# Performance work log

Measured on AMD Instinct MI355X. Metric: run time of the kernel, lower is better.

## Reference

```python
import jax, jax.numpy as jnp
import numpy as np

# ---- config (YOLOv4-style, TRAIN_SIZE=608, P2..P5) ----
STRIDES = (4.0, 8.0, 16.0, 32.0)
ANCHORS = np.array([
    [[12, 16], [19, 36], [40, 28], [36, 75]],
    [[36, 75], [76, 55], [72, 146], [142, 110]],
    [[72, 146], [142, 110], [192, 243], [459, 401]],
    [[142, 110], [192, 243], [300, 300], [459, 401]],
], dtype=np.float32)  # [LEVELS, NUM_ANCHORS, 2]
MAX_PROP = 100
SCORE_THRESH = 0.25
IOU_THRESH = 0.5


def decode_prediction(p, anchors, stride):
    # p: [b, A, h, w, 6] -> [b, A*h*w, 5] with xyxy + score
    b, A, h, w, _ = p.shape
    txy, twh, conf, cls = p[..., :2], p[..., 2:4], p[..., 4:5], p[..., 5:6]
    gx, gy = jnp.meshgrid(jnp.arange(w, dtype=p.dtype), jnp.arange(h, dtype=p.dtype))
    grid = jnp.stack([gx, gy], axis=-1)[None, None]  # [1,1,h,w,2]
    xy = (jax.nn.sigmoid(txy) + grid) * stride
    wh = jnp.exp(twh) * anchors[None, :, None, None, :]
    score = jax.nn.sigmoid(conf) * jax.nn.sigmoid(cls)
    x1y1 = xy - 0.5 * wh
    x2y2 = xy + 0.5 * wh
    out = jnp.concatenate([x1y1, x2y2, score], axis=-1)  # [b,A,h,w,5]
    return out.reshape(b, A * h * w, 5)


def _iou_one_vs_all(box, boxes):
    # box: [4], boxes: [N,4] (xyxy)
    lt = jnp.maximum(box[:2], boxes[:, :2])
    rb = jnp.minimum(box[2:], boxes[:, 2:])
    wh = jnp.maximum(rb - lt, 0.0)
    inter = wh[:, 0] * wh[:, 1]
    a1 = jnp.maximum(box[2] - box[0], 0.0) * jnp.maximum(box[3] - box[1], 0.0)
    a2 = jnp.maximum(boxes[:, 2] - boxes[:, 0], 0.0) * jnp.maximum(boxes[:, 3] - boxes[:, 1], 0.0)
    return inter / (a1 + a2 - inter + 1e-9)


def _nms_single(boxes, scores):
    # greedy NMS, padded to MAX_PROP with zero rows
    s0 = jnp.where(scores >= SCORE_THRESH, scores, 0.0)

    def step(s, _):
        i = jnp.argmax(s)
        sc = s[i]
        box = boxes[i]
        keep = sc > 0.0
        row = jnp.where(keep, jnp.concatenate([box, sc[None]]), jnp.zeros(5, boxes.dtype))
        iou = _iou_one_vs_all(box, boxes)
        s = jnp.where((iou > IOU_THRESH) & keep, 0.0, s)
        s = s.at[i].set(0.0)
        return s, row

    _, props = jax.lax.scan(step, s0, None, length=MAX_PROP)
    return props  # [MAX_PROP, 5]


def entry_stop_gradients(t, mask):
    # gradient flows only through entries where mask==1
    return jax.lax.stop_gradient(t) * (1.0 - mask) + t * mask


def _forward(p2, p3, p4, p5):
    anchors = jnp.asarray(ANCHORS)
    d2 = decode_prediction(p2, anchors[0], STRIDES[0])
    d3 = decode_prediction(p3, anchors[1], STRIDES[1])
    d4 = decode_prediction(p4, anchors[2], STRIDES[2])
    d5 = decode_prediction(p5, anchors[3], STRIDES[3])
    proposals = jnp.concatenate([d2, d3, d4, d5], axis=1)  # [b, N, 5]
    proposals = jax.vmap(lambda pr: _nms_single(pr[:, :4], pr[:, 4]))(proposals)  # [b, MAX_PROP, 5]
    mask = (jnp.sum(proposals[..., :4], axis=-1) != 0.0).astype(proposals.dtype)[..., None]
    return entry_stop_gradients(proposals, mask)


def setup_inputs() -> dict:
    key = jax.random.key(0)
    k2, k3, k4, k5 = jax.random.split(key, 4)
    b, A, ch = 32, 4, 6
    return {
        "p2": jax.random.normal(k2, (b, A, 152, 152, ch), dtype=jnp.float32),
        "p3": jax.random.normal(k3, (b, A, 76, 76, ch), dtype=jnp.float32),
        "p4": jax.random.normal(k4, (b, A, 38, 38, ch), dtype=jnp.float32),
        "p5": jax.random.normal(k5, (b, A, 19, 19, ch), dtype=jnp.float32),
    }


def reference(p2, p3, p4, p5):
    return _forward(p2, p3, p4, p5)
```

## Files before the change

kernel.cpp:

```cpp
#include <hip/hip_runtime.h>
#include <cstdint>
#include <cstddef>

typedef unsigned int u32;
typedef unsigned long long u64;

#define NTOT 122740
#define NQ   30685
#define NPAIR 61370
#define KTOP 1024
#define WIN  256
#define NBIN 4096
#define SCORE_T 0.25f
#define TBITS 0x3E800000u


#define WS_SCORES 524288

__device__ __forceinline__ float sigm(float x) { return 1.0f / (1.0f + expf(-x)); }

__device__ __forceinline__ int score_bin(u32 bits) {
  return min(4095, 1 + (int)((bits - TBITS) >> 12));
}

__device__ __forceinline__ u64 shfl_u64(u64 x, int src) {
  int lo = __shfl((int)(u32)x, src, 64);
  int hi = __shfl((int)(u32)(x >> 32), src, 64);
  return ((u64)(u32)hi << 32) | (u32)lo;
}

__device__ float4 decode_box_from_gidx(u32 gidx, int b,
    const float* __restrict__ p2, const float* __restrict__ p3,
    const float* __restrict__ p4, const float* __restrict__ p5)
{
  const float* p; int t, H, W; float stride;
  float aw0, ah0, aw1, ah1, aw2, ah2, aw3, ah3;
  if (gidx < 92416u) {
    p = p2 + (size_t)b * 92416 * 6; t = (int)gidx; H = 152; W = 152; stride = 4.0f;
    aw0=12.f; ah0=16.f; aw1=19.f; ah1=36.f; aw2=40.f; ah2=28.f; aw3=36.f; ah3=75.f;
  } else if (gidx < 115520u) {
    p = p3 + (size_t)b * 23104 * 6; t = (int)(gidx - 92416u); H = 76; W = 76; stride = 8.0f;
    aw0=36.f; ah0=75.f; aw1=76.f; ah1=55.f; aw2=72.f; ah2=146.f; aw3=142.f; ah3=110.f;
  } else if (gidx < 121296u) {
    p = p4 + (size_t)b * 5776 * 6; t = (int)(gidx - 115520u); H = 38; W = 38; stride = 16.0f;
    aw0=72.f; ah0=146.f; aw1=142.f; ah1=110.f; aw2=192.f; ah2=243.f; aw3=459.f; ah3=401.f;
  } else {
    p = p5 + (size_t)b * 1444 * 6; t = (int)(gidx - 121296u); H = 19; W = 19; stride = 32.0f;
    aw0=142.f; ah0=110.f; aw1=192.f; ah1=243.f; aw2=300.f; ah2=300.f; aw3=459.f; ah3=401.f;
  }
  int HW = H * W;
  int a = t / HW;
  int r = t - a * HW;
  int y = r / W;
  int x = r - y * W;
  const float* q = p + (size_t)t * 6;
  float2 t01 = *(const float2*)(q + 0);
  float2 t23 = *(const float2*)(q + 2);
  float cx = (sigm(t01.x) + (float)x) * stride;
  float cy = (sigm(t01.y) + (float)y) * stride;
  float aw = (a == 0) ? aw0 : (a == 1) ? aw1 : (a == 2) ? aw2 : aw3;
  float ah = (a == 0) ? ah0 : (a == 1) ? ah1 : (a == 2) ? ah2 : ah3;
  float bw = expf(t23.x) * aw;
  float bh = expf(t23.y) * ah;
  return make_float4(cx - 0.5f * bw, cy - 0.5f * bh, cx + 0.5f * bw, cy + 0.5f * bh);
}

__device__ __forceinline__ bool iou_gt(float4 A, float4 B) {
  float ltx = fmaxf(A.x, B.x), lty = fmaxf(A.y, B.y);
  float rbx = fminf(A.z, B.z), rby = fminf(A.w, B.w);
  float w = fmaxf(rbx - ltx, 0.0f), h = fmaxf(rby - lty, 0.0f);
  float inter = w * h;
  float a1 = fmaxf(A.z - A.x, 0.0f) * fmaxf(A.w - A.y, 0.0f);
  float a2 = fmaxf(B.z - B.x, 0.0f) * fmaxf(B.w - B.y, 0.0f);
  float iou = inter / (a1 + a2 - inter + 1e-9f);
  return iou > 0.5f;
}

__global__ __launch_bounds__(256)
void decode_score_hist(const float* __restrict__ p2, const float* __restrict__ p3,
                       const float* __restrict__ p4, const float* __restrict__ p5,
                       u32* __restrict__ scores, u32* __restrict__ hist)
{
  __shared__ u32 lhist[NBIN];
  const int tid = threadIdx.x;
  const int b = blockIdx.y;
  for (int i = tid; i < NBIN; i += 256) lhist[i] = 0u;
  __syncthreads();

  uint2* srow = (uint2*)(scores + (size_t)b * NTOT);
  const int pbase = blockIdx.x * 2048;
  #pragma unroll 2
  for (int k = 0; k < 8; ++k) {
    int P = pbase + k * 256 + tid;
    if (P < NPAIR) {
      int t0 = 2 * P;
      const float* p; int l0, LN;
      if (t0 < 92416)       { p = p2; l0 = t0;          LN = 92416; }
      else if (t0 < 115520) { p = p3; l0 = t0 - 92416;  LN = 23104; }
      else if (t0 < 121296) { p = p4; l0 = t0 - 115520; LN = 5776;  }
      else                  { p = p5; l0 = t0 - 121296; LN = 1444;  }
      const float* q = p + ((size_t)b * LN + (size_t)l0) * 6 + 4;
      float4 v1 = *(const float4*)(q);
      float4 v2 = *(const float4*)(q + 4);
      float s0 = sigm(v1.x) * sigm(v1.y);
      float s1 = sigm(v2.z) * sigm(v2.w);
      u32 b0 = (s0 >= SCORE_T) ? __float_as_uint(s0) : 0u;
      u32 b1 = (s1 >= SCORE_T) ? __float_as_uint(s1) : 0u;
      srow[P] = make_uint2(b0, b1);
      if (b0) atomicAdd(&lhist[score_bin(b0)], 1u);
      if (b1) atomicAdd(&lhist[score_bin(b1)], 1u);
    }
  }
  __syncthreads();
  u32* gh = hist + (size_t)b * NBIN;
  for (int i = tid; i < NBIN; i += 256) {
    u32 v = lhist[i];
    if (v) atomicAdd(&gh[i], v);
  }
}

__global__ __launch_bounds__(1024, 1)
void mega_kernel(const u32* __restrict__ scores, const u32* __restrict__ hist,
                 const float* __restrict__ p2, const float* __restrict__ p3,
                 const float* __restrict__ p4, const float* __restrict__ p5,
                 float* __restrict__ out)
{
  const int b = blockIdx.x;
  const int tid = threadIdx.x;

  __shared__ u32 sstart[NBIN];
  __shared__ u32 scur[NBIN];
  __shared__ u32 sscan[256];
  __shared__ u64 skey[KTOP];
  __shared__ u64 skey2[KTOP];
  __shared__ float4 sbox[WIN];
  __shared__ u64 smat[WIN * 4];
  __shared__ float4 selbox[100];
  __shared__ int s_misc[4];
  __shared__ int s_B, s_n;

  const u32* gh = hist + (size_t)b * NBIN;
  for (int i = tid; i < NBIN; i += 1024) scur[i] = gh[i];
  __syncthreads();

  u32 loc[16]; int base = 0;
  if (tid < 256) {
    base = tid * 16;
    u32 g = 0;
    #pragma unroll
    for (int k = 0; k < 16; ++k) { loc[k] = scur[base + k]; g += loc[k]; }
    sscan[tid] = g;
  }
  __syncthreads();
  for (int off = 1; off < 256; off <<= 1) {
    u32 v = 0;
    if (tid < 256) v = (tid + off < 256) ? sscan[tid + off] : 0u;
    __syncthreads();
    if (tid < 256) sscan[tid] += v;
    __syncthreads();
  }
  if (tid == 0 && sscan[0] <= (u32)KTOP) { s_B = 1; s_n = (int)sscan[0]; }
  if (tid < 256) {
    u32 nxt = (tid < 255) ? sscan[tid + 1] : 0u;
    if (sscan[tid] > (u32)KTOP && nxt <= (u32)KTOP) {
      u32 c = nxt; int Bv = base + 16; u32 nv = nxt;
      for (int k = 15; k >= 0; --k) {
        c += loc[k];
        if (c <= (u32)KTOP) { Bv = base + k; nv = c; } else break;
      }
      s_B = Bv; s_n = (int)nv;
    }
    u32 s = nxt;
    for (int k = 15; k >= 0; --k) { sstart[base + k] = s; s += loc[k]; }
  }
  __syncthreads();
  const int B = max(s_B, 1);
  const int n = min(s_n, KTOP);

  for (int i = tid; i < NBIN; i += 1024) scur[i] = sstart[i];
  skey[tid] = 0ull;
  skey2[tid] = 0ull;
  __syncthreads();

  {
    const uint4* sp = (const uint4*)(scores + (size_t)b * NTOT);
    #pragma unroll 1
    for (int kk = 0; kk < 8; ++kk) {
      int i0 = kk * 4096 + tid;
      uint4 v0, v1, v2, v3;
      bool g0 = (i0        < NQ), g1 = (i0 + 1024 < NQ);
      bool g2 = (i0 + 2048 < NQ), g3 = (i0 + 3072 < NQ);
      if (g0) v0 = sp[i0];
      if (g1) v1 = sp[i0 + 1024];
      if (g2) v2 = sp[i0 + 2048];
      if (g3) v3 = sp[i0 + 3072];
      #pragma unroll
      for (int q = 0; q < 4; ++q) {
        bool gq = (q == 0) ? g0 : (q == 1) ? g1 : (q == 2) ? g2 : g3;
        if (!gq) continue;
        uint4 v = (q == 0) ? v0 : (q == 1) ? v1 : (q == 2) ? v2 : v3;
        int ii = i0 + q * 1024;
        u32 c4[4] = { v.x, v.y, v.z, v.w };
        #pragma unroll
        for (int c = 0; c < 4; ++c) {
          u32 bits = c4[c];
          if (bits) {
            int bin = score_bin(bits);
            if (bin >= B) {
              u32 slot = atomicAdd(&scur[bin], 1u);
              if (slot < (u32)KTOP)
                skey[slot] = ((u64)bits << 32) | (u32)(~(u32)(4 * ii + c));
            }
          }
        }
      }
    }
  }
  __syncthreads();

  for (int s = tid; s < n; s += 1024) {
    u64 k = skey[s];
    int bin = score_bin((u32)(k >> 32));
    int st = (int)sstart[bin];
    int en = (int)scur[bin];
    u32 r = 0;
    for (int j = st; j < en; ++j) r += (skey[j] > k) ? 1u : 0u;
    skey2[st + r] = k;
  }
  __syncthreads();

  const int Wn = min(n, WIN);

  if (tid < WIN) {
    sbox[tid] = (tid < Wn) ? decode_box_from_gidx(~(u32)skey2[tid], b, p2, p3, p4, p5)
                           : make_float4(0.f, 0.f, 0.f, 0.f);
  }
  __syncthreads();

  {
    int row = tid & 255, word = tid >> 8;
    u64 bits = 0;
    if (row < Wn) {
      float4 A = sbox[row];
      int j0 = word * 64;
      int je = min(64, Wn - j0);
      for (int j = 0; j < je; ++j)
        if (iou_gt(A, sbox[j0 + j])) bits |= (1ull << j);
    }
    smat[word * 256 + row] = bits;
  }
  __syncthreads();

  if (tid < 64) {
    const int lane = tid;
    u64 m0[4], m1[4], m2[4], m3[4];
    #pragma unroll
    for (int w = 0; w < 4; ++w) {
      m0[w] = smat[w * 256 +   0 + lane];
      m1[w] = smat[w * 256 +  64 + lane];
      m2[w] = smat[w * 256 + 128 + lane];
      m3[w] = smat[w * 256 + 192 + lane];
    }
    u64 live[4];
    #pragma unroll
    for (int g2 = 0; g2 < 4; ++g2) {
      int lo = g2 * 64;
      live[g2] = (Wn >= lo + 64) ? ~0ull : (Wn > lo ? ((1ull << (Wn - lo)) - 1ull) : 0ull);
    }
    int sel = 0;
    #pragma unroll 1
    for (int w2 = 0; w2 < 4; ++w2) {
      while (live[w2] && sel < 100) {
        int j = (int)__ffsll(live[w2]) - 1;
        int p = (w2 << 6) + j;
        u64 r0, r1, r2, r3;
        if (w2 == 0)      { r0 = shfl_u64(m0[0], j); r1 = shfl_u64(m0[1], j); r2 = shfl_u64(m0[2], j); r3 = shfl_u64(m0[3], j); }
        else if (w2 == 1) { r0 = shfl_u64(m1[0], j); r1 = shfl_u64(m1[1], j); r2 = shfl_u64(m1[2], j); r3 = shfl_u64(m1[3], j); }
        else if (w2 == 2) { r0 = shfl_u64(m2[0], j); r1 = shfl_u64(m2[1], j); r2 = shfl_u64(m2[2], j); r3 = shfl_u64(m2[3], j); }
        else              { r0 = shfl_u64(m3[0], j); r1 = shfl_u64(m3[1], j); r2 = shfl_u64(m3[2], j); r3 = shfl_u64(m3[3], j); }
        live[0] &= ~r0; live[1] &= ~r1; live[2] &= ~r2; live[3] &= ~r3;
        live[w2] &= ~(1ull << j);
        if (lane == 0) {
          float4 box = sbox[p];
          u64 k = skey2[p];
          float sc = __uint_as_float((u32)(k >> 32));
          selbox[sel] = box;
          float* orow = out + (size_t)b * 500 + (size_t)sel * 5;
          orow[0] = box.x; orow[1] = box.y; orow[2] = box.z; orow[3] = box.w; orow[4] = sc;
        }
        sel++;
      }
    }
    if (lane == 0) {
      s_misc[2] = sel;
      s_misc[3] = (sel < 100 && n > WIN) ? 1 : 0;
    }
  }
  __syncthreads();

  if (s_misc[3]) {
    if (tid < 64) {
      const int lane = tid;
      int sel = s_misc[2];
      for (int p = WIN; p < n && sel < 100; ++p) {
        u64 k = skey2[p];
        float4 box = decode_box_from_gidx(~(u32)k, b, p2, p3, p4, p5);
        bool hit = false;
        if (lane < sel) hit = iou_gt(selbox[lane], box);
        if (lane + 64 < sel) hit = hit || iou_gt(selbox[lane + 64], box);
        u64 anyhit = __ballot(hit);
        if (anyhit == 0ull) {
          if (lane == 0) {
            selbox[sel] = box;
            float sc = __uint_as_float((u32)(k >> 32));
            float* orow = out + (size_t)b * 500 + (size_t)sel * 5;
            orow[0] = box.x; orow[1] = box.y; orow[2] = box.z; orow[3] = box.w; orow[4] = sc;
          }
          sel++;
        }
      }
      if (lane == 0) s_misc[2] = sel;
    }
  }
  __syncthreads();

  const int nsel = s_misc[2];
  for (int i = tid; i < (100 - nsel) * 5; i += 1024)
    out[(size_t)b * 500 + (size_t)nsel * 5 + i] = 0.0f;
}

extern "C" void kernel_launch(void* const* d_in, const int* in_sizes, int n_in,
                              void* d_out, int out_size, void* d_ws, size_t ws_size,
                              hipStream_t stream) {
  const float* p2 = (const float*)d_in[0];
  const float* p3 = (const float*)d_in[1];
  const float* p4 = (const float*)d_in[2];
  const float* p5 = (const float*)d_in[3];
  float* out = (float*)d_out;

  unsigned char* w = (unsigned char*)d_ws;
  u32* hist   = (u32*)w;
  u32* scores = (u32*)(w + WS_SCORES);

  hipMemsetAsync(hist, 0, 32 * NBIN * sizeof(u32), stream);
  decode_score_hist<<<dim3(30, 32), 256, 0, stream>>>(p2, p3, p4, p5, scores, hist);
  mega_kernel<<<32, 1024, 0, stream>>>(scores, hist, p2, p3, p4, p5, out);
}
```

Baseline: 184.6 us.

## Compact candidates into high/low score lists instead of dense score arrays

The decode kernel now appends above-threshold candidates to two compacted per-batch lists, split by score (at or above about 0.5 versus below), using wave-ballot aggregated atomics. It no longer writes a dense score array. The selection kernel then scans only the high list, plus the low list when the cutoff bin is low, instead of streaming all 122,740 scores per image. The histogram prefix scan is rewritten as a single-wave shuffle scan. The cost is global atomics on the append counters and a nondeterministic candidate order, which the later sort by key handles.

```diff
diff --git a/kernel.cpp b/kernel.cpp
--- a/kernel.cpp
+++ b/kernel.cpp
@@ -6,16 +6,20 @@
 typedef unsigned long long u64;
 
 #define NTOT 122740
-#define NQ   30685
 #define NPAIR 61370
 #define KTOP 1024
 #define WIN  256
 #define NBIN 4096
 #define SCORE_T 0.25f
 #define TBITS 0x3E800000u
-
-
-#define WS_SCORES 524288
+#define HSPLIT_BITS 0x3EFFF000u
+#define CSTRIDE 64
+#define CAP 30685
+
+
+#define WS_COUNTERS 524288
+#define WS_CANDH    532480
+#define WS_CANDL    8387840
 
 __device__ __forceinline__ float sigm(float x) { return 1.0f / (1.0f + expf(-x)); }
 
@@ -27,6 +31,22 @@
   int lo = __shfl((int)(u32)x, src, 64);
   int hi = __shfl((int)(u32)(x >> 32), src, 64);
   return ((u64)(u32)hi << 32) | (u32)lo;
+}
+
+__device__ __forceinline__ void wave_append(bool pred, u32 bits, u32 gidx,
+                                            u32* gcnt, uint2* glist, int lane)
+{
+  u64 m = __ballot(pred);
+  if (!m) return;
+  int leader = (int)__ffsll(m) - 1;
+  u32 cnt = (u32)__popcll(m);
+  u32 base = 0;
+  if (lane == leader) base = atomicAdd(gcnt, cnt);
+  base = (u32)__shfl((int)base, leader, 64);
+  if (pred) {
+    u32 pos = base + (u32)__popcll(m & ((1ull << lane) - 1ull));
+    if (pos < (u32)CAP) glist[pos] = make_uint2(bits, gidx);
+  }
 }
 
 __device__ float4 decode_box_from_gidx(u32 gidx, int b,
@@ -79,19 +99,25 @@
 __global__ __launch_bounds__(256)
 void decode_score_hist(const float* __restrict__ p2, const float* __restrict__ p3,
                        const float* __restrict__ p4, const float* __restrict__ p5,
-                       u32* __restrict__ scores, u32* __restrict__ hist)
+                       u32* __restrict__ hist, u32* __restrict__ counters,
+                       uint2* __restrict__ candH, uint2* __restrict__ candL)
 {
   __shared__ u32 lhist[NBIN];
   const int tid = threadIdx.x;
+  const int lane = tid & 63;
   const int b = blockIdx.y;
   for (int i = tid; i < NBIN; i += 256) lhist[i] = 0u;
   __syncthreads();
 
-  uint2* srow = (uint2*)(scores + (size_t)b * NTOT);
+  u32* gcH = counters + (size_t)b * CSTRIDE;
+  u32* gcL = gcH + 1;
+  uint2* gH = candH + (size_t)b * CAP;
+  uint2* gL = candL + (size_t)b * CAP;
+
   const int pbase = blockIdx.x * 2048;
-  #pragma unroll 2
   for (int k = 0; k < 8; ++k) {
     int P = pbase + k * 256 + tid;
+    u32 b0 = 0, b1 = 0, gi0 = 0, gi1 = 0;
     if (P < NPAIR) {
       int t0 = 2 * P;
       const float* p; int l0, LN;
@@ -99,17 +125,21 @@
       else if (t0 < 115520) { p = p3; l0 = t0 - 92416;  LN = 23104; }
       else if (t0 < 121296) { p = p4; l0 = t0 - 115520; LN = 5776;  }
       else                  { p = p5; l0 = t0 - 121296; LN = 1444;  }
-      const float* q = p + ((size_t)b * LN + (size_t)l0) * 6 + 4;
-      float4 v1 = *(const float4*)(q);
-      float4 v2 = *(const float4*)(q + 4);
-      float s0 = sigm(v1.x) * sigm(v1.y);
-      float s1 = sigm(v2.z) * sigm(v2.w);
-      u32 b0 = (s0 >= SCORE_T) ? __float_as_uint(s0) : 0u;
-      u32 b1 = (s1 >= SCORE_T) ? __float_as_uint(s1) : 0u;
-      srow[P] = make_uint2(b0, b1);
+      const float* q = p + ((size_t)b * LN + (size_t)l0) * 6;
+      float2 c0 = *(const float2*)(q + 4);
+      float2 c1 = *(const float2*)(q + 10);
+      float s0 = sigm(c0.x) * sigm(c0.y);
+      float s1 = sigm(c1.x) * sigm(c1.y);
+      b0 = (s0 >= SCORE_T) ? __float_as_uint(s0) : 0u;
+      b1 = (s1 >= SCORE_T) ? __float_as_uint(s1) : 0u;
+      gi0 = (u32)t0; gi1 = (u32)(t0 + 1);
       if (b0) atomicAdd(&lhist[score_bin(b0)], 1u);
       if (b1) atomicAdd(&lhist[score_bin(b1)], 1u);
     }
+    wave_append(b0 != 0u && b0 >= HSPLIT_BITS, b0, gi0, gcH, gH, lane);
+    wave_append(b0 != 0u && b0 <  HSPLIT_BITS, b0, gi0, gcL, gL, lane);
+    wave_append(b1 != 0u && b1 >= HSPLIT_BITS, b1, gi1, gcH, gH, lane);
+    wave_append(b1 != 0u && b1 <  HSPLIT_BITS, b1, gi1, gcL, gL, lane);
   }
   __syncthreads();
   u32* gh = hist + (size_t)b * NBIN;
@@ -120,7 +150,8 @@
 }
 
 __global__ __launch_bounds__(1024, 1)
-void mega_kernel(const u32* __restrict__ scores, const u32* __restrict__ hist,
+void mega_kernel(const u32* __restrict__ hist, const u32* __restrict__ counters,
+                 const uint2* __restrict__ candH, const uint2* __restrict__ candL,
                  const float* __restrict__ p2, const float* __restrict__ p3,
                  const float* __restrict__ p4, const float* __restrict__ p5,
                  float* __restrict__ out)
@@ -130,7 +161,6 @@
 
   __shared__ u32 sstart[NBIN];
   __shared__ u32 scur[NBIN];
-  __shared__ u32 sscan[256];
   __shared__ u64 skey[KTOP];
   __shared__ u64 skey2[KTOP];
   __shared__ float4 sbox[WIN];
@@ -139,80 +169,73 @@
   __shared__ int s_misc[4];
   __shared__ int s_B, s_n;
 
-  const u32* gh = hist + (size_t)b * NBIN;
-  for (int i = tid; i < NBIN; i += 1024) scur[i] = gh[i];
-  __syncthreads();
-
-  u32 loc[16]; int base = 0;
-  if (tid < 256) {
-    base = tid * 16;
-    u32 g = 0;
-    #pragma unroll
-    for (int k = 0; k < 16; ++k) { loc[k] = scur[base + k]; g += loc[k]; }
-    sscan[tid] = g;
-  }
-  __syncthreads();
-  for (int off = 1; off < 256; off <<= 1) {
-    u32 v = 0;
-    if (tid < 256) v = (tid + off < 256) ? sscan[tid + off] : 0u;
-    __syncthreads();
-    if (tid < 256) sscan[tid] += v;
-    __syncthreads();
-  }
-  if (tid == 0 && sscan[0] <= (u32)KTOP) { s_B = 1; s_n = (int)sscan[0]; }
-  if (tid < 256) {
-    u32 nxt = (tid < 255) ? sscan[tid + 1] : 0u;
-    if (sscan[tid] > (u32)KTOP && nxt <= (u32)KTOP) {
-      u32 c = nxt; int Bv = base + 16; u32 nv = nxt;
-      for (int k = 15; k >= 0; --k) {
-        c += loc[k];
-        if (c <= (u32)KTOP) { Bv = base + k; nv = c; } else break;
+  if (tid < 64) {
+    const uint4* gq = (const uint4*)(hist + (size_t)b * NBIN + (size_t)tid * 64);
+    u32 h[64];
+    #pragma unroll
+    for (int i = 0; i < 16; ++i) {
+      uint4 t = gq[i];
+      h[4*i] = t.x; h[4*i+1] = t.y; h[4*i+2] = t.z; h[4*i+3] = t.w;
+    }
+    u32 lsum = 0;
+    #pragma unroll
+    for (int k = 0; k < 64; ++k) lsum += h[k];
+    u32 S = lsum;
+    #pragma unroll
+    for (int off = 1; off < 64; off <<= 1) {
+      u32 v = (u32)__shfl_down((int)S, off, 64);
+      if (tid + off < 64) S += v;
+    }
+    u32 c = S - lsum;
+    int Bv = -1; u32 nv = 0;
+    for (int k = 63; k >= 0; --k) {
+      sstart[tid * 64 + k] = c;
+      c += h[k];
+      if (c <= (u32)KTOP) { Bv = tid * 64 + k; nv = c; }
+    }
+    scur[tid]      = (Bv < 0) ? 0xFFFFFFFFu : (u32)Bv;
+    scur[64 + tid] = nv;
+  } else {
+    for (int i = tid - 64; i < KTOP; i += 960) { skey[i] = 0ull; skey2[i] = 0ull; }
+  }
+  __syncthreads();
+  if (tid == 0) {
+    u32 bb = 0xFFFFFFFFu, nn = 0;
+    for (int l = 0; l < 64; ++l) {
+      u32 v = scur[l];
+      if (v < bb) { bb = v; nn = scur[64 + l]; }
+    }
+    if (bb == 0xFFFFFFFFu) { s_B = 4095; s_n = KTOP; }
+    else { s_B = max((int)bb, 1); s_n = (int)nn; }
+  }
+  __syncthreads();
+  const int B = s_B;
+  const int n = min(s_n, KTOP);
+
+  for (int i = tid; i < NBIN; i += 1024) scur[i] = sstart[i];
+  __syncthreads();
+
+  {
+    const int nH = min((int)counters[(size_t)b * CSTRIDE], CAP);
+    const uint2* src = candH + (size_t)b * CAP;
+    for (int i = tid; i < nH; i += 1024) {
+      uint2 e = src[i];
+      int bin = score_bin(e.x);
+      if (bin >= B) {
+        u32 slot = atomicAdd(&scur[bin], 1u);
+        if (slot < (u32)KTOP) skey[slot] = ((u64)e.x << 32) | (u32)(~e.y);
       }
-      s_B = Bv; s_n = (int)nv;
-    }
-    u32 s = nxt;
-    for (int k = 15; k >= 0; --k) { sstart[base + k] = s; s += loc[k]; }
-  }
-  __syncthreads();
-  const int B = max(s_B, 1);
-  const int n = min(s_n, KTOP);
-
-  for (int i = tid; i < NBIN; i += 1024) scur[i] = sstart[i];
-  skey[tid] = 0ull;
-  skey2[tid] = 0ull;
-  __syncthreads();
-
-  {
-    const uint4* sp = (const uint4*)(scores + (size_t)b * NTOT);
-    #pragma unroll 1
-    for (int kk = 0; kk < 8; ++kk) {
-      int i0 = kk * 4096 + tid;
-      uint4 v0, v1, v2, v3;
-      bool g0 = (i0        < NQ), g1 = (i0 + 1024 < NQ);
-      bool g2 = (i0 + 2048 < NQ), g3 = (i0 + 3072 < NQ);
-      if (g0) v0 = sp[i0];
-      if (g1) v1 = sp[i0 + 1024];
-      if (g2) v2 = sp[i0 + 2048];
-      if (g3) v3 = sp[i0 + 3072];
-      #pragma unroll
-      for (int q = 0; q < 4; ++q) {
-        bool gq = (q == 0) ? g0 : (q == 1) ? g1 : (q == 2) ? g2 : g3;
-        if (!gq) continue;
-        uint4 v = (q == 0) ? v0 : (q == 1) ? v1 : (q == 2) ? v2 : v3;
-        int ii = i0 + q * 1024;
-        u32 c4[4] = { v.x, v.y, v.z, v.w };
-        #pragma unroll
-        for (int c = 0; c < 4; ++c) {
-          u32 bits = c4[c];
-          if (bits) {
-            int bin = score_bin(bits);
-            if (bin >= B) {
-              u32 slot = atomicAdd(&scur[bin], 1u);
-              if (slot < (u32)KTOP)
-                skey[slot] = ((u64)bits << 32) | (u32)(~(u32)(4 * ii + c));
-            }
-          }
-        }
+    }
+  }
+  if (B < 2048) {
+    const int nL = min((int)counters[(size_t)b * CSTRIDE + 1], CAP);
+    const uint2* src = candL + (size_t)b * CAP;
+    for (int i = tid; i < nL; i += 1024) {
+      uint2 e = src[i];
+      int bin = score_bin(e.x);
+      if (bin >= B) {
+        u32 slot = atomicAdd(&scur[bin], 1u);
+        if (slot < (u32)KTOP) skey[slot] = ((u64)e.x << 32) | (u32)(~e.y);
       }
     }
   }
@@ -339,10 +362,14 @@
   float* out = (float*)d_out;
 
   unsigned char* w = (unsigned char*)d_ws;
-  u32* hist   = (u32*)w;
-  u32* scores = (u32*)(w + WS_SCORES);
-
-  hipMemsetAsync(hist, 0, 32 * NBIN * sizeof(u32), stream);
-  decode_score_hist<<<dim3(30, 32), 256, 0, stream>>>(p2, p3, p4, p5, scores, hist);
-  mega_kernel<<<32, 1024, 0, stream>>>(scores, hist, p2, p3, p4, p5, out);
-}
+  u32*   hist     = (u32*)w;
+  u32*   counters = (u32*)(w + WS_COUNTERS);
+  uint2* candH    = (uint2*)(w + WS_CANDH);
+  uint2* candL    = (uint2*)(w + WS_CANDL);
+
+  hipMemsetAsync(w, 0, WS_CANDH, stream);
+  decode_score_hist<<<dim3(30, 32), 256, 0, stream>>>(p2, p3, p4, p5,
+                                                      hist, counters, candH, candL);
+  mega_kernel<<<32, 1024, 0, stream>>>(hist, counters, candH, candL,
+                                       p2, p3, p4, p5, out);
+}
```

After: 205.4 us. 1.11x slower.
